# Kernel optimization log

Measured on AMD Instinct MI355X. Metric: run time of the kernel, lower is better.

## Reference

```python
import jax, jax.numpy as jnp
import numpy as np

N_NODES = 200000
DIM = 480  # 128x0e + 64x1e (x3) + 32x2e (x5) = 128 + 192 + 160
N_SEG = 4096


def setup_inputs() -> dict:
    key = jax.random.key(0)
    k1, k2 = jax.random.split(key)
    node_input = jax.random.normal(k1, (N_NODES, DIM), dtype=jnp.float32)
    labels = jax.random.randint(k2, (N_NODES,), 0, N_SEG, dtype=jnp.int64)
    return {"node_input": node_input, "labels": labels, "n_segments": N_SEG}


def reference(node_input, labels, n_segments):
    # The torch module loops over irrep blocks doing scatter-mean along dim 0.
    # Since the reduction axis (nodes) is independent of the per-block
    # narrow/reshape, the loop is mathematically one fused segment-mean over
    # the full feature dimension.
    sums = jax.ops.segment_sum(node_input, labels, num_segments=n_segments)
    counts = jax.ops.segment_sum(
        jnp.ones((node_input.shape[0],), dtype=node_input.dtype),
        labels, num_segments=n_segments)
    # torch_scatter 'mean' yields 0 for empty segments
    denom = jnp.maximum(counts, 1.0)[:, None]
    return sums / denom
```

## Files before the change

### kernel.cpp

```cpp
#include <hip/hip_runtime.h>

#define N_NODES 200000
#define DIM 480
#define N_SEG 4096
#define VEC (DIM / 4)
#define CHUNK 8

__global__ void hist_kernel(const int* __restrict__ labels,
                            int* __restrict__ counts, int n) {
    int i = blockIdx.x * blockDim.x + threadIdx.x;
    if (i < n) atomicAdd(&counts[labels[i]], 1);
}

__global__ void scan_kernel(const int* __restrict__ counts,
                            int* __restrict__ cursor) {
    __shared__ int part[256];
    int t = threadIdx.x;
    int local[16];
    int base = t * 16;
    int sum = 0;
#pragma unroll
    for (int i = 0; i < 16; ++i) { local[i] = counts[base + i]; sum += local[i]; }
    part[t] = sum;
    __syncthreads();
    for (int off = 1; off < 256; off <<= 1) {
        int add = (t >= off) ? part[t - off] : 0;
        __syncthreads();
        part[t] += add;
        __syncthreads();
    }
    int excl = (t == 0) ? 0 : part[t - 1];
#pragma unroll
    for (int i = 0; i < 16; ++i) { cursor[base + i] = excl; excl += local[i]; }
}

__global__ void scatter_kernel(const int* __restrict__ labels,
                               int* __restrict__ cursor,
                               int* __restrict__ sorted_idx, int n) {
    int i = blockIdx.x * blockDim.x + threadIdx.x;
    if (i < n) {
        int pos = atomicAdd(&cursor[labels[i]], 1);
        sorted_idx[pos] = i;
    }
}

__global__ __launch_bounds__(128) void gather_mean_kernel(
    const float* __restrict__ x,
    const int* __restrict__ sorted_idx,
    const int* __restrict__ counts,
    const int* __restrict__ cursor,
    float* __restrict__ out) {
    int s = blockIdx.x;
    int cnt = counts[s];
    int end = cursor[s];
    int start = end - cnt;
    int t = threadIdx.x;
    if (t >= VEC) return;

    float4 acc = make_float4(0.f, 0.f, 0.f, 0.f);
    if (cnt > 0) {
        for (int j = start; j < end; j += CHUNK) {
            int   idx[CHUNK];
            float w[CHUNK];
#pragma unroll
            for (int k = 0; k < CHUNK; ++k) {
                int jj = j + k;
                w[k]   = (jj < end) ? 1.0f : 0.0f;
                idx[k] = sorted_idx[(jj < end) ? jj : start];
            }
            float4 v[CHUNK];
#pragma unroll
            for (int k = 0; k < CHUNK; ++k) {
                const float4* row = (const float4*)(x + (size_t)idx[k] * DIM);
                v[k] = row[t];
            }
#pragma unroll
            for (int k = 0; k < CHUNK; ++k) {
                acc.x = fmaf(w[k], v[k].x, acc.x);
                acc.y = fmaf(w[k], v[k].y, acc.y);
                acc.z = fmaf(w[k], v[k].z, acc.z);
                acc.w = fmaf(w[k], v[k].w, acc.w);
            }
        }
    }
    float inv = (cnt > 0) ? (1.0f / (float)cnt) : 0.0f;
    float4 r = make_float4(acc.x * inv, acc.y * inv, acc.z * inv, acc.w * inv);
    ((float4*)(out + (size_t)s * DIM))[t] = r;
}

extern "C" void kernel_launch(void* const* d_in, const int* in_sizes, int n_in,
                              void* d_out, int out_size, void* d_ws, size_t ws_size,
                              hipStream_t stream) {
    const float* x      = (const float*)d_in[0];
    const int*   labels = (const int*)d_in[1];
    float* out = (float*)d_out;

    int* counts     = (int*)d_ws;
    int* cursor     = counts + N_SEG;
    int* sorted_idx = cursor + N_SEG;

    hipMemsetAsync(counts, 0, N_SEG * sizeof(int), stream);

    hist_kernel<<<(N_NODES + 255) / 256, 256, 0, stream>>>(labels, counts, N_NODES);
    scan_kernel<<<1, 256, 0, stream>>>(counts, cursor);
    scatter_kernel<<<(N_NODES + 255) / 256, 256, 0, stream>>>(labels, cursor,
                                                              sorted_idx, N_NODES);
    gather_mean_kernel<<<N_SEG, 128, 0, stream>>>(x, sorted_idx, counts, cursor, out);
}
```

Baseline: 546.1 us.

## Record per-node rank in histogram and split segment rows across two thread slots

The histogram pass now stores each node's atomic rank, so the scatter pass writes sorted indices without a second round of atomics. The gather-mean kernel now uses 256 threads per segment: two 128-lane slots each accumulate alternate chunks of rows, and the partial sums are combined through shared memory before the mean is written. This aims to remove the second atomic pass and to put more loads in flight per segment. In exchange it adds a rank buffer to the workspace, a block barrier, and half-idle lanes in the final reduction.

```diff
diff --git a/kernel.cpp b/kernel.cpp
--- a/kernel.cpp
+++ b/kernel.cpp
@@ -5,15 +5,17 @@
 #define N_SEG 4096
 #define VEC (DIM / 4)
 #define CHUNK 8
+#define ROWSLOTS 2
 
 __global__ void hist_kernel(const int* __restrict__ labels,
-                            int* __restrict__ counts, int n) {
+                            int* __restrict__ counts,
+                            int* __restrict__ rank, int n) {
     int i = blockIdx.x * blockDim.x + threadIdx.x;
-    if (i < n) atomicAdd(&counts[labels[i]], 1);
+    if (i < n) rank[i] = atomicAdd(&counts[labels[i]], 1);
 }
 
 __global__ void scan_kernel(const int* __restrict__ counts,
-                            int* __restrict__ cursor) {
+                            int* __restrict__ offsets) {
     __shared__ int part[256];
     int t = threadIdx.x;
     int local[16];
@@ -31,40 +33,41 @@
     }
     int excl = (t == 0) ? 0 : part[t - 1];
 #pragma unroll
-    for (int i = 0; i < 16; ++i) { cursor[base + i] = excl; excl += local[i]; }
+    for (int i = 0; i < 16; ++i) { offsets[base + i] = excl; excl += local[i]; }
 }
 
 __global__ void scatter_kernel(const int* __restrict__ labels,
-                               int* __restrict__ cursor,
+                               const int* __restrict__ offsets,
+                               const int* __restrict__ rank,
                                int* __restrict__ sorted_idx, int n) {
     int i = blockIdx.x * blockDim.x + threadIdx.x;
-    if (i < n) {
-        int pos = atomicAdd(&cursor[labels[i]], 1);
-        sorted_idx[pos] = i;
-    }
+    if (i < n) sorted_idx[offsets[labels[i]] + rank[i]] = i;
 }
 
-__global__ __launch_bounds__(128) void gather_mean_kernel(
+__global__ __launch_bounds__(256) void gather_mean_kernel(
     const float* __restrict__ x,
     const int* __restrict__ sorted_idx,
     const int* __restrict__ counts,
-    const int* __restrict__ cursor,
+    const int* __restrict__ offsets,
     float* __restrict__ out) {
     int s = blockIdx.x;
     int cnt = counts[s];
-    int end = cursor[s];
-    int start = end - cnt;
+    int start = offsets[s];
+    int end = start + cnt;
     int t = threadIdx.x;
-    if (t >= VEC) return;
+    int slot = t >> 7;
+    int lane = t & 127;
+
+    __shared__ float4 red[VEC];
 
     float4 acc = make_float4(0.f, 0.f, 0.f, 0.f);
-    if (cnt > 0) {
-        for (int j = start; j < end; j += CHUNK) {
+    if (lane < VEC) {
+        for (int j0 = start + slot * CHUNK; j0 < end; j0 += ROWSLOTS * CHUNK) {
             int   idx[CHUNK];
             float w[CHUNK];
 #pragma unroll
             for (int k = 0; k < CHUNK; ++k) {
-                int jj = j + k;
+                int jj = j0 + k;
                 w[k]   = (jj < end) ? 1.0f : 0.0f;
                 idx[k] = sorted_idx[(jj < end) ? jj : start];
             }
@@ -72,7 +75,7 @@
 #pragma unroll
             for (int k = 0; k < CHUNK; ++k) {
                 const float4* row = (const float4*)(x + (size_t)idx[k] * DIM);
-                v[k] = row[t];
+                v[k] = row[lane];
             }
 #pragma unroll
             for (int k = 0; k < CHUNK; ++k) {
@@ -83,9 +86,19 @@
             }
         }
     }
-    float inv = (cnt > 0) ? (1.0f / (float)cnt) : 0.0f;
-    float4 r = make_float4(acc.x * inv, acc.y * inv, acc.z * inv, acc.w * inv);
-    ((float4*)(out + (size_t)s * DIM))[t] = r;
+
+    if (slot == 1 && lane < VEC) red[lane] = acc;
+    __syncthreads();
+    if (slot == 0 && lane < VEC) {
+        float4 o = red[lane];
+        float inv = (cnt > 0) ? (1.0f / (float)cnt) : 0.0f;
+        float4 r;
+        r.x = (acc.x + o.x) * inv;
+        r.y = (acc.y + o.y) * inv;
+        r.z = (acc.z + o.z) * inv;
+        r.w = (acc.w + o.w) * inv;
+        ((float4*)(out + (size_t)s * DIM))[lane] = r;
+    }
 }
 
 extern "C" void kernel_launch(void* const* d_in, const int* in_sizes, int n_in,
@@ -96,14 +109,18 @@
     float* out = (float*)d_out;
 
     int* counts     = (int*)d_ws;
-    int* cursor     = counts + N_SEG;
-    int* sorted_idx = cursor + N_SEG;
+    int* offsets    = counts + N_SEG;
+    int* rank       = offsets + N_SEG;
+    int* sorted_idx = rank + N_NODES;
 
     hipMemsetAsync(counts, 0, N_SEG * sizeof(int), stream);
 
-    hist_kernel<<<(N_NODES + 255) / 256, 256, 0, stream>>>(labels, counts, N_NODES);
-    scan_kernel<<<1, 256, 0, stream>>>(counts, cursor);
-    scatter_kernel<<<(N_NODES + 255) / 256, 256, 0, stream>>>(labels, cursor,
-                                                              sorted_idx, N_NODES);
-    gather_mean_kernel<<<N_SEG, 128, 0, stream>>>(x, sorted_idx, counts, cursor, out);
+    hist_kernel<<<(N_NODES + 255) / 256, 256, 0, stream>>>(labels, counts, rank,
+                                                           N_NODES);
+    scan_kernel<<<1, 256, 0, stream>>>(counts, offsets);
+    scatter_kernel<<<(N_NODES + 255) / 256, 256, 0, stream>>>(labels, offsets,
+                                                              rank, sorted_idx,
+                                                              N_NODES);
+    gather_mean_kernel<<<N_SEG, 256, 0, stream>>>(x, sorted_idx, counts, offsets,
+                                                  out);
 }
```

After: 530.8 us. 1.03x faster.
